# Performance work log

Hardware: AMD Instinct MI355X
Metric: run time of the kernel (lower is better)

Reference implementation:

```python
import jax, jax.numpy as jnp
import numpy as np

B, DIM, H, W = 8, 384, 64, 64
HEADS = 8
D = DIM // HEADS            # 48, per-head channel dim
DH = D // 2                 # 24
D2 = D // 3 * 2             # 32, conv_up hidden width (ratio=3)


def setup_inputs() -> dict:
    key = jax.random.key(0)
    ks = jax.random.split(key, 12)
    rn = lambda k, s, sc=0.05: jax.random.normal(k, s, dtype=jnp.float32) * sc
    return {
        "x": rn(ks[0], (B, DIM, H, W), 1.0),
        "w_qkv": rn(ks[1], (3 * DIM, DIM)),          # 1x1 conv dim->3dim, no bias
        "w_dw": rn(ks[2], (3 * DIM, 1, 3, 3)),       # depthwise 3x3, groups=3dim
        "temperature": jnp.ones((HEADS, 1, 1), jnp.float32),
        "w_ar": rn(ks[3], (1, D)),                   # conv_attn_right
        "w_vr": rn(ks[4], (DH, D)),                  # conv_v_right
        "w_up1": rn(ks[5], (D2, DH)),                # conv_up[0]
        "b_up1": jnp.zeros((D2,), jnp.float32),
        "ln_g": jnp.ones((D2, HEADS, 1), jnp.float32),   # LayerNorm([D2, 8, 1])
        "ln_b": jnp.zeros((D2, HEADS, 1), jnp.float32),
        "w_up2": rn(ks[6], (D, D2)),                 # conv_up[3]
        "b_up2": jnp.zeros((D,), jnp.float32),
        "w_al": rn(ks[7], (DH, D)),                  # conv_attn_left
        "w_vl": rn(ks[8], (DH, D)),                  # conv_v_left
        "w_proj": rn(ks[9], (DIM, HEADS)),           # project_out: Conv2d(heads, dim, 1)
    }


def reference(x, w_qkv, w_dw, temperature, w_ar, w_vr, w_up1, b_up1,
              ln_g, ln_b, w_up2, b_up2, w_al, w_vl, w_proj):
    b, c, h, w = x.shape
    hw = h * w
    # qkv = dwconv3x3(conv1x1(x)); the torch module computes this identically in
    # both spatial_pool and channel_pool, so compute once.
    qkv = jnp.einsum('oc,bchw->bohw', w_qkv, x)
    qkv = jax.lax.conv_general_dilated(
        qkv, w_dw, window_strides=(1, 1), padding='SAME',
        feature_group_count=3 * c, dimension_numbers=('NCHW', 'OIHW', 'NCHW'))
    q, k, v = jnp.split(qkv, 3, axis=1)
    hsplit = lambda t: t.reshape(b, HEADS, D, hw)        # 'b (head c) h w -> b head c (h w)'
    q, k, v = hsplit(q), hsplit(k), hsplit(v)
    l2n = lambda t: t / jnp.maximum(jnp.linalg.norm(t, axis=-1, keepdims=True), 1e-12)
    # elementwise q*k attention, temperature-scaled, softmax over spatial (hw)
    attn = jax.nn.softmax(l2n(q) * l2n(k) * temperature, axis=-1)   # [b,heads,D,hw]

    # ---- spatial_pool branch (produces channel gate) ----
    input_x = jnp.einsum('od,bhdn->bhon', w_vr, v)                  # [b,heads,DH,hw]
    cmask = jax.nn.softmax(jnp.einsum('od,bhdn->bhon', w_ar, attn), axis=-1)  # [b,heads,1,hw]
    ctx = jnp.einsum('bhin,bhjn->bhji', cmask, input_x)             # [b,heads,DH,1]
    ctx = ctx.transpose(0, 2, 1, 3)                                 # [b,DH,heads,1]
    t = jnp.einsum('op,bphl->bohl', w_up1, ctx) + b_up1[None, :, None, None]  # [b,D2,8,1]
    mu = t.mean(axis=(1, 2, 3), keepdims=True)
    var = t.var(axis=(1, 2, 3), keepdims=True)
    t = (t - mu) / jnp.sqrt(var + 1e-5) * ln_g[None] + ln_b[None]
    t = jax.nn.relu(t)
    t = jnp.einsum('op,bphl->bohl', w_up2, t) + b_up2[None, :, None, None]    # [b,D,8,1]
    # torch .view(b, head*d, 1, 1) on a [b, d, head, 1] tensor: plain reshape
    mask_ch = jax.nn.sigmoid(t).reshape(b, c, 1, 1)
    out_spatial = x * mask_ch

    # ---- channel_pool branch (produces spatial gate) ----
    g_x = jnp.einsum('od,bhdn->bhon', w_al, attn)                   # [b,heads,DH,hw]
    avg_x = jax.nn.softmax(g_x.mean(axis=-1), axis=-1)              # [b,heads,DH]
    theta_x = jnp.einsum('od,bhdn->bhon', w_vl, v)                  # [b,heads,DH,hw]
    mask_sp = jax.nn.sigmoid(jnp.einsum('bho,bhon->bhn', avg_x, theta_x))
    mask_sp = mask_sp.reshape(b, HEADS, h, w)
    mask_sp = jnp.einsum('oh,bhxy->boxy', w_proj, mask_sp)          # project_out
    out_channel = x * mask_sp

    return out_spatial + out_channel
```

## Files before the change

kernel.cpp:

```cpp
#include <hip/hip_runtime.h>
#include <math.h>
#include <stdint.h>

#define B_     8
#define DIM_   384
#define HEADS_ 8
#define D_     48
#define DH_    24
#define D2_    32
#define HW_    4096
#define IMG    64
#define CH3    1152

typedef __attribute__((ext_vector_type(8))) __bf16   bf16x8;
typedef __attribute__((ext_vector_type(4))) float    f32x4;
typedef __attribute__((ext_vector_type(8))) unsigned short u16x8;

__device__ __forceinline__ float b2f(unsigned short h){
  union { uint32_t u; float f; } v; v.u = ((uint32_t)h) << 16; return v.f;
}
__device__ __forceinline__ unsigned short f2b(float f){
  return __builtin_bit_cast(unsigned short, (__bf16)f);
}

__device__ __forceinline__ float wred_sum(float v){
#pragma unroll
  for (int m = 32; m; m >>= 1) v += __shfl_xor(v, m);
  return v;
}
template<int OP>
__device__ __forceinline__ float block_red(float v, float* lds){
  if (OP == 0) v = wred_sum(v);
  else if (OP == 1){
#pragma unroll
    for (int m = 32; m; m >>= 1) v = fmaxf(v, __shfl_xor(v, m));
  } else {
#pragma unroll
    for (int m = 32; m; m >>= 1) v = fminf(v, __shfl_xor(v, m));
  }
  const int lane = threadIdx.x & 63;
  const int wid  = threadIdx.x >> 6;
  __syncthreads();
  if (lane == 0) lds[wid] = v;
  __syncthreads();
  const int nw = blockDim.x >> 6;
  float r = lds[0];
  for (int i = 1; i < nw; ++i){
    float o = lds[i];
    if (OP == 0) r += o; else if (OP == 1) r = fmaxf(r, o); else r = fminf(r, o);
  }
  return r;
}

__device__ __forceinline__ void block_red4(float& s0, float& s1, float& mx, float& mn,
                                           float* lds ){
#pragma unroll
  for (int m = 32; m; m >>= 1){
    s0 += __shfl_xor(s0, m);
    s1 += __shfl_xor(s1, m);
    mx = fmaxf(mx, __shfl_xor(mx, m));
    mn = fminf(mn, __shfl_xor(mn, m));
  }
  const int lane = threadIdx.x & 63;
  const int wid  = threadIdx.x >> 6;
  __syncthreads();
  if (lane == 0){
    lds[wid*4+0] = s0; lds[wid*4+1] = s1; lds[wid*4+2] = mx; lds[wid*4+3] = mn;
  }
  __syncthreads();
  s0 = lds[0] + lds[4] + lds[8]  + lds[12];
  s1 = lds[1] + lds[5] + lds[9]  + lds[13];
  mx = fmaxf(fmaxf(lds[2], lds[6]), fmaxf(lds[10], lds[14]));
  mn = fminf(fminf(lds[3], lds[7]), fminf(lds[11], lds[15]));
}

__device__ __forceinline__ void dwplane16(const unsigned short* __restrict__ plane,
                                          const float* w9, int y, int x0, float* acc16){
#pragma unroll
  for (int j = 0; j < 16; ++j) acc16[j] = 0.f;
#pragma unroll
  for (int dy = -1; dy <= 1; ++dy){
    const int yy = y + dy;
    if ((unsigned)yy >= (unsigned)IMG) continue;
    const unsigned short* rp = plane + yy * IMG;
    u16x8 C0 = *reinterpret_cast<const u16x8*>(rp + x0);
    u16x8 C1 = *reinterpret_cast<const u16x8*>(rp + x0 + 8);
    float rw[18];
    rw[0]  = (x0 > 0)  ? b2f(rp[x0 - 1])  : 0.f;
    rw[17] = (x0 < 48) ? b2f(rp[x0 + 16]) : 0.f;
#pragma unroll
    for (int j = 0; j < 8; ++j){ rw[1+j] = b2f(C0[j]); rw[9+j] = b2f(C1[j]); }
    const float w0 = w9[(dy+1)*3], w1 = w9[(dy+1)*3+1], w2 = w9[(dy+1)*3+2];
#pragma unroll
    for (int j = 0; j < 16; ++j)
      acc16[j] = fmaf(rw[j], w0, fmaf(rw[j+1], w1, fmaf(rw[j+2], w2, acc16[j])));
  }
}

__global__ __launch_bounds__(256)
void k_prep2(const float* __restrict__ x, const float* __restrict__ w,
             unsigned short* __restrict__ xT, unsigned short* __restrict__ wb){
  __shared__ unsigned short Ts[64][66];
  const int t = threadIdx.x;
  if (blockIdx.x < 432){
    const int i = (blockIdx.x * 256 + t) * 4;
    float4 v = *reinterpret_cast<const float4*>(w + i);
    wb[i+0] = f2b(v.x); wb[i+1] = f2b(v.y); wb[i+2] = f2b(v.z); wb[i+3] = f2b(v.w);
    return;
  }
  const int id = blockIdx.x - 432;
  const int bz = id / 384;
  const int r2 = id % 384;
  const int by = r2 / 64, bx = r2 % 64;
  const float* xb = x + ((size_t)bz * DIM_ + by * 64) * HW_ + bx * 64;
#pragma unroll
  for (int rr = 0; rr < 4; ++rr){
    const int r = (t >> 4) + rr * 16;
    const int c = (t & 15) * 4;
    float4 v = *reinterpret_cast<const float4*>(xb + (size_t)r * HW_ + c);
    Ts[r][c+0] = f2b(v.x); Ts[r][c+1] = f2b(v.y); Ts[r][c+2] = f2b(v.z); Ts[r][c+3] = f2b(v.w);
  }
  __syncthreads();
  const int rn = t >> 2, kc = (t & 3) * 16;
  unsigned short* yb = xT + ((size_t)bz * HW_ + bx * 64 + rn) * DIM_ + by * 64 + kc;
  u16x8 o0, o1;
#pragma unroll
  for (int j = 0; j < 8; ++j){ o0[j] = Ts[kc + j][rn]; o1[j] = Ts[kc + 8 + j][rn]; }
  *reinterpret_cast<u16x8*>(yb)     = o0;
  *reinterpret_cast<u16x8*>(yb + 8) = o1;
}

__global__ __launch_bounds__(512, 4)
void k_gemm(const unsigned short* __restrict__ wb, const unsigned short* __restrict__ xT,
            unsigned short* __restrict__ qkv){
  const int b  = blockIdx.z;
  const int m0 = blockIdx.y * 128;
  const int n0 = blockIdx.x * 128;
  __shared__ unsigned short As[2][128 * 64];
  __shared__ unsigned short Bs[2][128 * 64];
  const int t = threadIdx.x;
  const int lane = t & 63;
  const int fr = lane & 15;
  const int ld = lane >> 4;
  const int w = t >> 6;
  const int wr = w >> 1, wc = w & 1;
  f32x4 acc[2][4];
#pragma unroll
  for (int i = 0; i < 2; ++i)
#pragma unroll
    for (int j = 0; j < 4; ++j) acc[i][j] = (f32x4){0.f,0.f,0.f,0.f};

  const unsigned short* Ag = wb + (size_t)m0 * DIM_;
  const unsigned short* Bg = xT + ((size_t)b * HW_ + n0) * DIM_;

  auto stage = [&](int buf, int k0){
#pragma unroll
    for (int i = 0; i < 2; ++i){
      const int q = i * 512 + t;
      const int qb = q & ~63;
      const int r = q >> 3, c = q & 7;
      const int cs = c ^ (r & 7);
      __builtin_amdgcn_global_load_lds(
        (const __attribute__((address_space(1))) void*)(Ag + (size_t)r * DIM_ + k0 + cs * 8),
        (__attribute__((address_space(3))) void*)(&As[buf][qb * 8]), 16, 0, 0);
    }
#pragma unroll
    for (int i = 0; i < 2; ++i){
      const int q = i * 512 + t;
      const int qb = q & ~63;
      const int r = q >> 3, c = q & 7;
      const int cs = c ^ (r & 7);
      __builtin_amdgcn_global_load_lds(
        (const __attribute__((address_space(1))) void*)(Bg + (size_t)r * DIM_ + k0 + cs * 8),
        (__attribute__((address_space(3))) void*)(&Bs[buf][qb * 8]), 16, 0, 0);
    }
  };

  stage(0, 0);
  for (int it = 0; it < 6; ++it){
    const int cur = it & 1;
    if (it < 5){
      stage(cur ^ 1, (it + 1) * 64);
      asm volatile("s_waitcnt vmcnt(4)" ::: "memory");
    } else {
      asm volatile("s_waitcnt vmcnt(0)" ::: "memory");
    }
    __builtin_amdgcn_s_barrier();
    asm volatile("" ::: "memory");
#pragma unroll
    for (int ks = 0; ks < 2; ++ks){
      bf16x8 af[2], bfr[4];
#pragma unroll
      for (int mi = 0; mi < 2; ++mi){
        const int row = wr * 32 + mi * 16 + fr;
        const int cc = (ks * 4 + ld) ^ (row & 7);
        af[mi] = *reinterpret_cast<const bf16x8*>(&As[cur][row * 64 + cc * 8]);
      }
#pragma unroll
      for (int ni = 0; ni < 4; ++ni){
        const int row = wc * 64 + ni * 16 + fr;
        const int cc = (ks * 4 + ld) ^ (row & 7);
        bfr[ni] = *reinterpret_cast<const bf16x8*>(&Bs[cur][row * 64 + cc * 8]);
      }
#pragma unroll
      for (int mi = 0; mi < 2; ++mi)
#pragma unroll
        for (int ni = 0; ni < 4; ++ni)
          acc[mi][ni] = __builtin_amdgcn_mfma_f32_16x16x32_bf16(af[mi], bfr[ni], acc[mi][ni], 0, 0, 0);
    }
    asm volatile("" ::: "memory");
    __builtin_amdgcn_s_barrier();
  }
  unsigned short* yb = qkv + ((size_t)b * CH3 + m0) * HW_ + n0;
#pragma unroll
  for (int mi = 0; mi < 2; ++mi){
    const int rbase = wr * 32 + mi * 16 + (lane >> 4) * 4;
#pragma unroll
    for (int ni = 0; ni < 4; ++ni){
      const int col = wc * 64 + ni * 16 + (lane & 15);
#pragma unroll
      for (int r = 0; r < 4; ++r)
        yb[(size_t)(rbase + r) * HW_ + col] = f2b(acc[mi][ni][r]);
    }
  }
}

__global__ __launch_bounds__(256)
void k_dwqkv(unsigned short* __restrict__ qkv, const float* __restrict__ w_dw,
             const float* __restrict__ temperature, const float* __restrict__ w_ar,
             float* __restrict__ prm){
  const int pc = blockIdx.x;
  const int ch = pc % DIM_;
  const int b  = pc / DIM_;
  const int d  = ch % D_;
  const int head = ch / D_;
  unsigned short* qp = qkv + ((size_t)b * CH3 + ch) * HW_;
  const unsigned short* kp = qp + (size_t)DIM_ * HW_;
  unsigned short* vp = qp + (size_t)(2 * DIM_) * HW_;
  const int t  = threadIdx.x;
  const int y  = t >> 2;
  const int x0 = (t & 3) * 16;
  float wq9[9], wk9[9], wv9[9];
#pragma unroll
  for (int i = 0; i < 9; ++i){
    wq9[i] = w_dw[ch*9+i];
    wk9[i] = w_dw[(DIM_+ch)*9+i];
    wv9[i] = w_dw[(2*DIM_+ch)*9+i];
  }
  float aq[16], ak[16], av[16];
  dwplane16(qp, wq9, y, x0, aq);
  dwplane16(kp, wk9, y, x0, ak);
  dwplane16(vp, wv9, y, x0, av);
  __shared__ float lds[16];
  float pr[16];
  float sq = 0.f, sk = 0.f, pmx = -3.0e38f, pmn = 3.0e38f;
#pragma unroll
  for (int j = 0; j < 16; ++j){
    sq = fmaf(aq[j], aq[j], sq);
    sk = fmaf(ak[j], ak[j], sk);
    pr[j] = aq[j] * ak[j];
    pmx = fmaxf(pmx, pr[j]); pmn = fminf(pmn, pr[j]);
  }
  block_red4(sq, sk, pmx, pmn, lds);
  const float nq = fmaxf(sqrtf(sq), 1e-12f);
  const float nk = fmaxf(sqrtf(sk), 1e-12f);
  const float c  = temperature[head] / (nq * nk);
  const float m  = (c >= 0.f) ? c * pmx : c * pmn;
  float se = 0.f;
#pragma unroll
  for (int j = 0; j < 16; ++j) se += __expf(fmaf(c, pr[j], -m));
  se = block_red<0>(se, lds);
  u16x8 o0, o1;
#pragma unroll
  for (int j = 0; j < 8; ++j){ o0[j] = f2b(pr[j]); o1[j] = f2b(pr[8+j]); }
  *reinterpret_cast<u16x8*>(qp + (size_t)y * IMG + x0)     = o0;
  *reinterpret_cast<u16x8*>(qp + (size_t)y * IMG + x0 + 8) = o1;
#pragma unroll
  for (int j = 0; j < 8; ++j){ o0[j] = f2b(av[j]); o1[j] = f2b(av[8+j]); }
  *reinterpret_cast<u16x8*>(vp + (size_t)y * IMG + x0)     = o0;
  *reinterpret_cast<u16x8*>(vp + (size_t)y * IMG + x0 + 8) = o1;
  if (t == 0){
    prm[pc*4+0] = c;
    prm[pc*4+1] = m;
    prm[pc*4+2] = w_ar[d] / se;
    prm[pc*4+3] = 0.f;
  }
}

__global__ __launch_bounds__(256)
void k_attn_a(const unsigned short* __restrict__ dqkv, const float* __restrict__ prm,
              float* __restrict__ abuf){
  const int bh   = blockIdx.y;
  const int head = bh & 7, b = bh >> 3;
  const int t = threadIdx.x;
  const int px0 = (blockIdx.x * 256 + t) * 2;
  __shared__ float4 pc[D_];
  if (t < D_) pc[t] = reinterpret_cast<const float4*>(prm)[bh * D_ + t];
  __syncthreads();
  const unsigned short* pbase = dqkv + ((size_t)b * CH3 + head * D_) * HW_ + px0;
  float a0 = 0.f, a1 = 0.f;
  for (int d = 0; d < D_; ++d){
    const uint32_t pv = *reinterpret_cast<const uint32_t*>(pbase + (size_t)d * HW_);
    const float4 pp = pc[d];
    a0 = fmaf(pp.z, __expf(fmaf(pp.x, b2f((unsigned short)pv), -pp.y)), a0);
    a1 = fmaf(pp.z, __expf(fmaf(pp.x, b2f((unsigned short)(pv >> 16)), -pp.y)), a1);
  }
  float2 o; o.x = a0; o.y = a1;
  *reinterpret_cast<float2*>(abuf + (size_t)bh * HW_ + px0) = o;
}

__global__ __launch_bounds__(256)
void k_vctx(const unsigned short* __restrict__ dqkv, const float* __restrict__ abuf,
            float* __restrict__ vctx){
  const int bid  = blockIdx.x;
  const int d    = bid % D_;
  const int head = (bid / D_) % HEADS_;
  const int b    = bid / (D_ * HEADS_);
  const unsigned short* vp = dqkv + ((size_t)b * CH3 + 2*DIM_ + head*D_ + d) * HW_;
  const float* am = abuf + ((size_t)(b * HEADS_ + head)) * HW_;
  __shared__ float lds[16];
  const int t = threadIdx.x;
  float a16[16];
#pragma unroll
  for (int i = 0; i < 4; ++i)
    *reinterpret_cast<float4*>(&a16[i*4]) =
      *reinterpret_cast<const float4*>(am + t*16 + i*4);
  float mx = -3.0e38f;
#pragma unroll
  for (int j = 0; j < 16; ++j) mx = fmaxf(mx, a16[j]);
  mx = block_red<1>(mx, lds);
  float e16[16];
  float sl = 0.f;
#pragma unroll
  for (int j = 0; j < 16; ++j){ e16[j] = __expf(a16[j] - mx); sl += e16[j]; }
  const float S = block_red<0>(sl, lds);
  const float inv = 1.f / S;
  u16x8 v0 = *reinterpret_cast<const u16x8*>(vp + t * 16);
  u16x8 v1 = *reinterpret_cast<const u16x8*>(vp + t * 16 + 8);
  float s = 0.f;
#pragma unroll
  for (int j = 0; j < 8; ++j) s = fmaf(e16[j] * inv,   b2f(v0[j]), s);
#pragma unroll
  for (int j = 0; j < 8; ++j) s = fmaf(e16[8+j] * inv, b2f(v1[j]), s);
  s = block_red<0>(s, lds);
  if (t == 0) vctx[bid] = s;
}

__global__ __launch_bounds__(256)
void k_spmask(const unsigned short* __restrict__ dqkv, const float* __restrict__ w_al,
              const float* __restrict__ w_vl, float* __restrict__ spb){
  const int bh   = blockIdx.y;
  const int head = bh & 7, b = bh >> 3;
  const int t = threadIdx.x;
  const int px0 = (blockIdx.x * 256 + t) * 2;
  __shared__ float u[D_];
  __shared__ float avg[DH_];
  if (t < DH_){
    float s = 0.f;
    for (int d = 0; d < D_; ++d) s += w_al[t*D_ + d];
    avg[t] = s * (1.f/(float)HW_);
  }
  __syncthreads();
  if (t == 0){
    float mx = avg[0];
    for (int o = 1; o < DH_; ++o) mx = fmaxf(mx, avg[o]);
    float s = 0.f;
    for (int o = 0; o < DH_; ++o){ avg[o] = expf(avg[o]-mx); s += avg[o]; }
    const float inv = 1.f/s;
    for (int o = 0; o < DH_; ++o) avg[o] *= inv;
  }
  __syncthreads();
  if (t < D_){
    float s = 0.f;
    for (int o = 0; o < DH_; ++o) s = fmaf(avg[o], w_vl[o*D_ + t], s);
    u[t] = s;
  }
  __syncthreads();
  const unsigned short* vb = dqkv + ((size_t)b * CH3 + 2*DIM_ + head*D_) * HW_ + px0;
  float a0 = 0.f, a1 = 0.f;
  for (int d = 0; d < D_; ++d){
    const uint32_t vv = *reinterpret_cast<const uint32_t*>(vb + (size_t)d * HW_);
    const float ud = u[d];
    a0 = fmaf(ud, b2f((unsigned short)vv), a0);
    a1 = fmaf(ud, b2f((unsigned short)(vv >> 16)), a1);
  }
  float2 o;
  o.x = 1.f/(1.f + __expf(-a0));
  o.y = 1.f/(1.f + __expf(-a1));
  *reinterpret_cast<float2*>(spb + (size_t)bh * HW_ + px0) = o;
}

__global__ __launch_bounds__(256)
void k_maskch(const float* __restrict__ vctx, const float* __restrict__ w_vr,
              const float* __restrict__ w_up1, const float* __restrict__ b_up1,
              const float* __restrict__ ln_g, const float* __restrict__ ln_b,
              const float* __restrict__ w_up2, const float* __restrict__ b_up2,
              float* __restrict__ mch){
  const int b = blockIdx.x;
  const int t = threadIdx.x;
  __shared__ float vc[HEADS_*D_];
  __shared__ float cx[HEADS_*DH_];
  __shared__ float t1[D2_*HEADS_];
  __shared__ float lds[16];
  for (int i = t; i < HEADS_*D_; i += 256) vc[i] = vctx[b*HEADS_*D_ + i];
  __syncthreads();
  if (t < HEADS_*DH_){
    const int head = t / DH_, o = t % DH_;
    float s = 0.f;
    for (int d = 0; d < D_; ++d) s = fmaf(w_vr[o*D_+d], vc[head*D_+d], s);
    cx[head*DH_+o] = s;
  }
  __syncthreads();
  const int o2 = t >> 3, hh = t & 7;
  float val = b_up1[o2];
  for (int o = 0; o < DH_; ++o) val = fmaf(w_up1[o2*DH_+o], cx[hh*DH_+o], val);
  const float mu  = block_red<0>(val, lds) * (1.f/256.f);
  const float dv  = val - mu;
  const float var = block_red<0>(dv*dv, lds) * (1.f/256.f);
  float yv = dv / sqrtf(var + 1e-5f);
  yv = fmaf(yv, ln_g[t], ln_b[t]);
  yv = fmaxf(yv, 0.f);
  t1[t] = yv;
  __syncthreads();
  for (int idx = t; idx < D_*HEADS_; idx += 256){
    const int d = idx >> 3, head2 = idx & 7;
    float s = b_up2[d];
    for (int o = 0; o < D2_; ++o) s = fmaf(w_up2[d*D2_+o], t1[o*HEADS_+head2], s);
    mch[b*DIM_ + idx] = 1.f/(1.f + __expf(-s));
  }
}

__global__ __launch_bounds__(256)
void k_out(const float* __restrict__ x, const float* __restrict__ spb,
           const float* __restrict__ mch, const float* __restrict__ w_proj,
           float* __restrict__ out){
  const int b  = blockIdx.z;
  const int c0 = blockIdx.y * 16;
  const int n  = blockIdx.x * 1024 + threadIdx.x * 4;
  float4 sv[8];
#pragma unroll
  for (int h = 0; h < 8; ++h)
    sv[h] = *reinterpret_cast<const float4*>(spb + ((size_t)(b*8+h))*HW_ + n);
  for (int ci = 0; ci < 16; ++ci){
    const int c = c0 + ci;
    const float g = mch[b*DIM_ + c];
    float4 gv; gv.x = g; gv.y = g; gv.z = g; gv.w = g;
#pragma unroll
    for (int h = 0; h < 8; ++h){
      const float wp = w_proj[c*8+h];
      gv.x = fmaf(wp, sv[h].x, gv.x); gv.y = fmaf(wp, sv[h].y, gv.y);
      gv.z = fmaf(wp, sv[h].z, gv.z); gv.w = fmaf(wp, sv[h].w, gv.w);
    }
    const size_t off = ((size_t)b*DIM_ + c)*HW_ + n;
    float4 xv = *reinterpret_cast<const float4*>(x + off);
    xv.x *= gv.x; xv.y *= gv.y; xv.z *= gv.z; xv.w *= gv.w;
    *reinterpret_cast<float4*>(out + off) = xv;
  }
}

extern "C" void kernel_launch(void* const* d_in, const int* in_sizes, int n_in,
                              void* d_out, int out_size, void* d_ws, size_t ws_size,
                              hipStream_t stream) {
  const float* x      = (const float*)d_in[0];
  const float* w_qkv  = (const float*)d_in[1];
  const float* w_dw   = (const float*)d_in[2];
  const float* temp   = (const float*)d_in[3];
  const float* w_ar   = (const float*)d_in[4];
  const float* w_vr   = (const float*)d_in[5];
  const float* w_up1  = (const float*)d_in[6];
  const float* b_up1  = (const float*)d_in[7];
  const float* ln_g   = (const float*)d_in[8];
  const float* ln_b   = (const float*)d_in[9];
  const float* w_up2  = (const float*)d_in[10];
  const float* b_up2  = (const float*)d_in[11];
  const float* w_al   = (const float*)d_in[12];
  const float* w_vl   = (const float*)d_in[13];
  const float* w_proj = (const float*)d_in[14];
  float* out = (float*)d_out;

  unsigned short* qkvb = (unsigned short*)d_ws;
  unsigned short* xT   = qkvb + (size_t)B_*CH3*HW_;
  unsigned short* wb   = xT + (size_t)B_*HW_*DIM_;
  float* prm  = (float*)(wb + (size_t)CH3*DIM_);
  float* abuf = prm + 4*B_*HEADS_*D_;
  float* vctx = abuf + (size_t)B_*HEADS_*HW_;
  float* spb  = vctx + B_*HEADS_*D_;
  float* mch  = spb + (size_t)B_*HEADS_*HW_;

  k_prep2<<<dim3(432 + B_*384), 256, 0, stream>>>(x, w_qkv, xT, wb);
  k_gemm<<<dim3(HW_/128, CH3/128, B_), 512, 0, stream>>>(wb, xT, qkvb);
  k_dwqkv<<<dim3(B_*DIM_), 256, 0, stream>>>(qkvb, w_dw, temp, w_ar, prm);
  k_attn_a<<<dim3(8, B_*HEADS_), 256, 0, stream>>>(qkvb, prm, abuf);
  k_vctx<<<dim3(B_*HEADS_*D_), 256, 0, stream>>>(qkvb, abuf, vctx);
  k_spmask<<<dim3(8, B_*HEADS_), 256, 0, stream>>>(qkvb, w_al, w_vl, spb);
  k_maskch<<<dim3(B_), 256, 0, stream>>>(vctx, w_vr, w_up1, b_up1, ln_g, ln_b,
                                         w_up2, b_up2, mch);
  k_out<<<dim3(HW_/1024, DIM_/16, B_), 256, 0, stream>>>(x, spb, mch, w_proj, out);
}
```

Baseline: 242.4 us.

## Use analytic softmax bound and prefetch dwconv rows with shuffle halos

Replaces the per-plane max/min reduction with the Cauchy-Schwarz bound |T|, since c·q·k never exceeds |T| after L2 normalisation. This shrinks the block reduction from four values to two and moves the exp-sum after the stores. All nine row vectors for q, k and v are now loaded up front, out-of-range rows are masked through zeroed weights, and the left and right halo pixels come from lane shuffles instead of scalar global loads. The launch bound now hints at 4 blocks per CU, which increases register pressure from the prefetched rows, and the looser softmax shift could lose precision when the true max is far below |T|.

New measurement: 221.1 us. -8.8%, faster.

```diff
diff --git a/kernel.cpp b/kernel.cpp
--- a/kernel.cpp
+++ b/kernel.cpp
@@ -52,49 +52,19 @@
   return r;
 }
 
-__device__ __forceinline__ void block_red4(float& s0, float& s1, float& mx, float& mn,
-                                           float* lds ){
+__device__ __forceinline__ void block_red2(float& s0, float& s1, float* lds){
 #pragma unroll
   for (int m = 32; m; m >>= 1){
     s0 += __shfl_xor(s0, m);
     s1 += __shfl_xor(s1, m);
-    mx = fmaxf(mx, __shfl_xor(mx, m));
-    mn = fminf(mn, __shfl_xor(mn, m));
   }
   const int lane = threadIdx.x & 63;
   const int wid  = threadIdx.x >> 6;
   __syncthreads();
-  if (lane == 0){
-    lds[wid*4+0] = s0; lds[wid*4+1] = s1; lds[wid*4+2] = mx; lds[wid*4+3] = mn;
-  }
-  __syncthreads();
-  s0 = lds[0] + lds[4] + lds[8]  + lds[12];
-  s1 = lds[1] + lds[5] + lds[9]  + lds[13];
-  mx = fmaxf(fmaxf(lds[2], lds[6]), fmaxf(lds[10], lds[14]));
-  mn = fminf(fminf(lds[3], lds[7]), fminf(lds[11], lds[15]));
-}
-
-__device__ __forceinline__ void dwplane16(const unsigned short* __restrict__ plane,
-                                          const float* w9, int y, int x0, float* acc16){
-#pragma unroll
-  for (int j = 0; j < 16; ++j) acc16[j] = 0.f;
-#pragma unroll
-  for (int dy = -1; dy <= 1; ++dy){
-    const int yy = y + dy;
-    if ((unsigned)yy >= (unsigned)IMG) continue;
-    const unsigned short* rp = plane + yy * IMG;
-    u16x8 C0 = *reinterpret_cast<const u16x8*>(rp + x0);
-    u16x8 C1 = *reinterpret_cast<const u16x8*>(rp + x0 + 8);
-    float rw[18];
-    rw[0]  = (x0 > 0)  ? b2f(rp[x0 - 1])  : 0.f;
-    rw[17] = (x0 < 48) ? b2f(rp[x0 + 16]) : 0.f;
-#pragma unroll
-    for (int j = 0; j < 8; ++j){ rw[1+j] = b2f(C0[j]); rw[9+j] = b2f(C1[j]); }
-    const float w0 = w9[(dy+1)*3], w1 = w9[(dy+1)*3+1], w2 = w9[(dy+1)*3+2];
-#pragma unroll
-    for (int j = 0; j < 16; ++j)
-      acc16[j] = fmaf(rw[j], w0, fmaf(rw[j+1], w1, fmaf(rw[j+2], w2, acc16[j])));
-  }
+  if (lane == 0){ lds[wid*2] = s0; lds[wid*2+1] = s1; }
+  __syncthreads();
+  s0 = lds[0] + lds[2] + lds[4] + lds[6];
+  s1 = lds[1] + lds[3] + lds[5] + lds[7];
 }
 
 __global__ __launch_bounds__(256)
@@ -225,7 +195,7 @@
   }
 }
 
-__global__ __launch_bounds__(256)
+__global__ __launch_bounds__(256, 4)
 void k_dwqkv(unsigned short* __restrict__ qkv, const float* __restrict__ w_dw,
              const float* __restrict__ temperature, const float* __restrict__ w_ar,
              float* __restrict__ prm){
@@ -247,29 +217,63 @@
     wk9[i] = w_dw[(DIM_+ch)*9+i];
     wv9[i] = w_dw[(2*DIM_+ch)*9+i];
   }
+  bool rok[3];
+  size_t roff[3];
+#pragma unroll
+  for (int r = 0; r < 3; ++r){
+    const int yy = y + r - 1;
+    rok[r]  = (unsigned)yy < (unsigned)IMG;
+    roff[r] = (size_t)(rok[r] ? yy : 0) * IMG + x0;
+  }
+  u16x8 Q0[3], Q1[3], K0[3], K1[3], V0[3], V1[3];
+#pragma unroll
+  for (int r = 0; r < 3; ++r){
+    Q0[r] = *reinterpret_cast<const u16x8*>(qp + roff[r]);
+    Q1[r] = *reinterpret_cast<const u16x8*>(qp + roff[r] + 8);
+    K0[r] = *reinterpret_cast<const u16x8*>(kp + roff[r]);
+    K1[r] = *reinterpret_cast<const u16x8*>(kp + roff[r] + 8);
+    V0[r] = *reinterpret_cast<const u16x8*>(vp + roff[r]);
+    V1[r] = *reinterpret_cast<const u16x8*>(vp + roff[r] + 8);
+  }
+  const int xg = t & 3;
+  auto accum = [&](const u16x8* C0, const u16x8* C1, const float* w9, float* a16){
+#pragma unroll
+    for (int j = 0; j < 16; ++j) a16[j] = 0.f;
+#pragma unroll
+    for (int r = 0; r < 3; ++r){
+      const float g  = rok[r] ? 1.f : 0.f;
+      const float w0 = w9[r*3+0] * g, w1 = w9[r*3+1] * g, w2 = w9[r*3+2] * g;
+      const uint32_t lw = __shfl_up  ((int)__builtin_bit_cast(uint4, C1[r]).w, 1);
+      const uint32_t rw0= __shfl_down((int)__builtin_bit_cast(uint4, C0[r]).x, 1);
+      float rw[18];
+      rw[0]  = (xg > 0) ? b2f((unsigned short)(lw >> 16)) : 0.f;
+      rw[17] = (xg < 3) ? b2f((unsigned short)rw0)        : 0.f;
+#pragma unroll
+      for (int j = 0; j < 8; ++j){ rw[1+j] = b2f(C0[r][j]); rw[9+j] = b2f(C1[r][j]); }
+#pragma unroll
+      for (int j = 0; j < 16; ++j)
+        a16[j] = fmaf(rw[j], w0, fmaf(rw[j+1], w1, fmaf(rw[j+2], w2, a16[j])));
+    }
+  };
   float aq[16], ak[16], av[16];
-  dwplane16(qp, wq9, y, x0, aq);
-  dwplane16(kp, wk9, y, x0, ak);
-  dwplane16(vp, wv9, y, x0, av);
-  __shared__ float lds[16];
+  accum(Q0, Q1, wq9, aq);
+  accum(K0, K1, wk9, ak);
+  accum(V0, V1, wv9, av);
+  __shared__ float lds[8];
   float pr[16];
-  float sq = 0.f, sk = 0.f, pmx = -3.0e38f, pmn = 3.0e38f;
+  float sq = 0.f, sk = 0.f;
 #pragma unroll
   for (int j = 0; j < 16; ++j){
     sq = fmaf(aq[j], aq[j], sq);
     sk = fmaf(ak[j], ak[j], sk);
     pr[j] = aq[j] * ak[j];
-    pmx = fmaxf(pmx, pr[j]); pmn = fminf(pmn, pr[j]);
-  }
-  block_red4(sq, sk, pmx, pmn, lds);
+  }
+  block_red2(sq, sk, lds);
+  const float T  = temperature[head];
   const float nq = fmaxf(sqrtf(sq), 1e-12f);
   const float nk = fmaxf(sqrtf(sk), 1e-12f);
-  const float c  = temperature[head] / (nq * nk);
-  const float m  = (c >= 0.f) ? c * pmx : c * pmn;
-  float se = 0.f;
-#pragma unroll
-  for (int j = 0; j < 16; ++j) se += __expf(fmaf(c, pr[j], -m));
-  se = block_red<0>(se, lds);
+  const float c  = T / (nq * nk);
+  const float m  = fabsf(T);
   u16x8 o0, o1;
 #pragma unroll
   for (int j = 0; j < 8; ++j){ o0[j] = f2b(pr[j]); o1[j] = f2b(pr[8+j]); }
@@ -279,6 +283,10 @@
   for (int j = 0; j < 8; ++j){ o0[j] = f2b(av[j]); o1[j] = f2b(av[8+j]); }
   *reinterpret_cast<u16x8*>(vp + (size_t)y * IMG + x0)     = o0;
   *reinterpret_cast<u16x8*>(vp + (size_t)y * IMG + x0 + 8) = o1;
+  float se = 0.f;
+#pragma unroll
+  for (int j = 0; j < 16; ++j) se += __expf(fmaf(c, pr[j], -m));
+  se = block_red<0>(se, lds);
   if (t == 0){
     prm[pc*4+0] = c;
     prm[pc*4+1] = m;
```
